# Optimization experiments

Hardware: AMD Instinct MI355X
Metric: run time of the kernel (lower is better)

## Reference

```python
import jax, jax.numpy as jnp
import numpy as np

B, S, D = 4, 1024, 512
E = 16            # num_skills
DH = 4 * D        # expert hidden
DS = 2 * D        # shared expert hidden
TOP_K = 2
TEMP = 0.7
SHARED_SCALE = 0.25
EPS = 1e-5

def layer_norm(x, g, b):
    mu = jnp.mean(x, axis=-1, keepdims=True)
    var = jnp.mean(jnp.square(x - mu), axis=-1, keepdims=True)
    return (x - mu) * jax.lax.rsqrt(var + EPS) * g + b

def setup_inputs() -> dict:
    key = jax.random.key(0)
    ks = jax.random.split(key, 12)
    s = 0.02
    return {
        "x": jax.random.normal(ks[0], (B, S, D), jnp.float32),
        # input LayerNorm
        "ln_in_g": jnp.ones((D,), jnp.float32),
        "ln_in_b": jnp.zeros((D,), jnp.float32),
        # router Linear(D -> E)
        "router_w": jax.random.normal(ks[1], (D, E), jnp.float32) * s,
        "router_b": jnp.zeros((E,), jnp.float32),
        # experts: Linear(D->DH), SiLU, Linear(DH->D), stacked over E
        "ew1": jax.random.normal(ks[2], (E, D, DH), jnp.float32) * s,
        "eb1": jnp.zeros((E, DH), jnp.float32),
        "ew2": jax.random.normal(ks[3], (E, DH, D), jnp.float32) * s,
        "eb2": jnp.zeros((E, D), jnp.float32),
        # shared expert: Linear(D->DS), SiLU, Linear(DS->D), *0.25
        "sw1": jax.random.normal(ks[4], (D, DS), jnp.float32) * s,
        "sb1": jnp.zeros((DS,), jnp.float32),
        "sw2": jax.random.normal(ks[5], (DS, D), jnp.float32) * s,
        "sb2": jnp.zeros((D,), jnp.float32),
        # final ff: LayerNorm, Linear(D->4D), SiLU, Linear(4D->D)
        "ff_ln_g": jnp.ones((D,), jnp.float32),
        "ff_ln_b": jnp.zeros((D,), jnp.float32),
        "ff_w1": jax.random.normal(ks[6], (D, DH), jnp.float32) * s,
        "ff_b1": jnp.zeros((DH,), jnp.float32),
        "ff_w2": jax.random.normal(ks[7], (DH, D), jnp.float32) * s,
        "ff_b2": jnp.zeros((D,), jnp.float32),
    }

def reference(x, ln_in_g, ln_in_b, router_w, router_b,
              ew1, eb1, ew2, eb2, sw1, sb1, sw2, sb2,
              ff_ln_g, ff_ln_b, ff_w1, ff_b1, ff_w2, ff_b2):
    h = layer_norm(x, ln_in_g, ln_in_b)                      # [B,S,D]
    # router: softmax(Linear(h)/temperature)
    gate = jax.nn.softmax((h @ router_w + router_b) / TEMP, axis=-1)  # [B,S,E]
    vals, idx = jax.lax.top_k(gate, TOP_K)                   # [B,S,K]
    # combine weights per expert: sum_j vals_j * onehot(idx_j)
    comb = jnp.sum(jax.nn.one_hot(idx, E, dtype=h.dtype) * vals[..., None], axis=-2)  # [B,S,E]
    # all-expert forward (same math as masked loop in the original)
    eh = jax.nn.silu(jnp.einsum('bsd,edh->ebsh', h, ew1) + eb1[:, None, None, :])      # [E,B,S,DH]
    ey = jnp.einsum('ebsh,ehd->ebsd', eh, ew2) + eb2[:, None, None, :]                  # [E,B,S,D]
    mix = jnp.einsum('bse,ebsd->bsd', comb, ey)              # top-k weighted combine
    shared = (jax.nn.silu(h @ sw1 + sb1) @ sw2 + sb2) * SHARED_SCALE
    moe_out = mix + shared                                   # h after MoE
    fh = layer_norm(moe_out, ff_ln_g, ff_ln_b)
    ff_out = jax.nn.silu(fh @ ff_w1 + ff_b1) @ ff_w2 + ff_b2
    return x + moe_out + ff_out
```

## Files before the change

### kernel.cpp

```cpp
#include <hip/hip_runtime.h>
#include <stdint.h>

#define T_TOK 4096
#define DIM   512
#define NEXP  16
#define DHID  2048
#define DSH   1024
#define ROWSCAP 10240
#define MAXTILES 80

typedef __bf16 bf16x8 __attribute__((ext_vector_type(8)));
typedef float  f32x4  __attribute__((ext_vector_type(4)));
typedef unsigned short usv8 __attribute__((ext_vector_type(8)));

__device__ __forceinline__ unsigned short f2b(float f) {
  union { float f; unsigned int u; } un; un.f = f;
  unsigned int u = un.u + 0x7fffu + ((un.u >> 16) & 1u);
  return (unsigned short)(u >> 16);
}
__device__ __forceinline__ float b2f(unsigned short u) {
  union { unsigned int u; float f; } un; un.u = ((unsigned int)u) << 16; return un.f;
}

__device__ __forceinline__ void async16(void* lds, const void* gp) {
  __builtin_amdgcn_global_load_lds(
      (const __attribute__((address_space(1))) unsigned int*)gp,
      (__attribute__((address_space(3))) unsigned int*)lds, 16, 0, 0);
}

__device__ __forceinline__ void transpose64(
    const float* __restrict__ s, unsigned short* __restrict__ d, int R, int C,
    int tx, int ty, float* tile) {
  const int tid = threadIdx.x;
  const int c0 = tx * 64, r0 = ty * 64;
  const int r = tid >> 4, j4 = (tid & 15) * 4;
#pragma unroll
  for (int p = 0; p < 4; ++p) {
    const int row = r + p * 16;
    const float4 v = *(const float4*)&s[(size_t)(r0 + row) * C + c0 + j4];
    tile[row * 65 + j4 + 0] = v.x;
    tile[row * 65 + j4 + 1] = v.y;
    tile[row * 65 + j4 + 2] = v.z;
    tile[row * 65 + j4 + 3] = v.w;
  }
  __syncthreads();
  const int jj = tid & 7, cc = tid >> 3;
#pragma unroll
  for (int p = 0; p < 2; ++p) {
    const int c = cc + p * 32;
    usv8 u;
#pragma unroll
    for (int i = 0; i < 8; ++i) u[i] = f2b(tile[(jj * 8 + i) * 65 + c]);
    *(usv8*)&d[(size_t)(c0 + c) * R + r0 + jj * 8] = u;
  }
}

__global__ __launch_bounds__(256) void prep_kernel(
    const float* __restrict__ x, const float* __restrict__ g, const float* __restrict__ b,
    const float* __restrict__ rw, const float* __restrict__ rb,
    unsigned short* __restrict__ hbuf, int* __restrict__ comb_idx, float* __restrict__ comb_w,
    int* __restrict__ counts,
    const float* __restrict__ ew1, const float* __restrict__ ew2,
    const float* __restrict__ sw1, const float* __restrict__ sw2,
    const float* __restrict__ fw1, const float* __restrict__ fw2,
    unsigned short* __restrict__ ew1T, unsigned short* __restrict__ ew2T,
    unsigned short* __restrict__ sw1T, unsigned short* __restrict__ sw2T,
    unsigned short* __restrict__ fw1T, unsigned short* __restrict__ fw2T) {
  __shared__ float tile[64 * 65];
  __shared__ int hist[NEXP];
  const int id = blockIdx.x;
  if (id >= 1024) {
    int id2 = id - 1024;
    const float* s; unsigned short* d; int R, C, t, tx, ty;
    if (id2 < 4096)      { int bm = id2 >> 8; t = id2 & 255; R = 512;  C = 2048;
                           s = ew1 + (size_t)bm * R * C; d = ew1T + (size_t)bm * R * C;
                           tx = t & 31; ty = t >> 5; }
    else if (id2 < 8192) { id2 -= 4096; int bm = id2 >> 8; t = id2 & 255; R = 2048; C = 512;
                           s = ew2 + (size_t)bm * R * C; d = ew2T + (size_t)bm * R * C;
                           tx = t & 7;  ty = t >> 3; }
    else if (id2 < 8320) { t = id2 - 8192; R = 512;  C = 1024; s = sw1; d = sw1T; tx = t & 15; ty = t >> 4; }
    else if (id2 < 8448) { t = id2 - 8320; R = 1024; C = 512;  s = sw2; d = sw2T; tx = t & 7;  ty = t >> 3; }
    else if (id2 < 8704) { t = id2 - 8448; R = 512;  C = 2048; s = fw1; d = fw1T; tx = t & 31; ty = t >> 5; }
    else                 { t = id2 - 8704; R = 2048; C = 512;  s = fw2; d = fw2T; tx = t & 7;  ty = t >> 3; }
    transpose64(s, d, R, C, tx, ty, tile);
    return;
  }
  const int wid = threadIdx.x >> 6, lane = threadIdx.x & 63;
  const int t = id * 4 + wid;
  if (threadIdx.x < NEXP) hist[threadIdx.x] = 0;
  __syncthreads();

  const float4* xr = (const float4*)(x + (size_t)t * DIM);
  const float4 va = xr[lane], vb = xr[lane + 64];
  float s = (va.x + va.y) + (va.z + va.w) + ((vb.x + vb.y) + (vb.z + vb.w));
#pragma unroll
  for (int o = 32; o; o >>= 1) s += __shfl_xor(s, o, 64);
  const float mu = s * (1.f / DIM);
  float da[4] = {va.x - mu, va.y - mu, va.z - mu, va.w - mu};
  float db[4] = {vb.x - mu, vb.y - mu, vb.z - mu, vb.w - mu};
  float q = (da[0]*da[0] + da[1]*da[1]) + (da[2]*da[2] + da[3]*da[3]) +
            ((db[0]*db[0] + db[1]*db[1]) + (db[2]*db[2] + db[3]*db[3]));
#pragma unroll
  for (int o = 32; o; o >>= 1) q += __shfl_xor(q, o, 64);
  const float rs = rsqrtf(q * (1.f / DIM) + 1e-5f);
  const float4 ga = ((const float4*)g)[lane], gb4 = ((const float4*)g)[lane + 64];
  const float4 ba = ((const float4*)b)[lane], bb4 = ((const float4*)b)[lane + 64];
  float ha[4], hbv[4];
  ha[0] = da[0] * rs * ga.x + ba.x;  ha[1] = da[1] * rs * ga.y + ba.y;
  ha[2] = da[2] * rs * ga.z + ba.z;  ha[3] = da[3] * rs * ga.w + ba.w;
  hbv[0] = db[0] * rs * gb4.x + bb4.x;  hbv[1] = db[1] * rs * gb4.y + bb4.y;
  hbv[2] = db[2] * rs * gb4.z + bb4.z;  hbv[3] = db[3] * rs * gb4.w + bb4.w;
  ushort4 ua = {f2b(ha[0]), f2b(ha[1]), f2b(ha[2]), f2b(ha[3])};
  ushort4 ub = {f2b(hbv[0]), f2b(hbv[1]), f2b(hbv[2]), f2b(hbv[3])};
  ((ushort4*)(hbuf + (size_t)t * DIM))[lane] = ua;
  ((ushort4*)(hbuf + (size_t)t * DIM))[lane + 64] = ub;

  float p[NEXP];
#pragma unroll
  for (int e = 0; e < NEXP; ++e) p[e] = 0.f;
  const int col0 = lane * 4;
#pragma unroll
  for (int half = 0; half < 2; ++half) {
#pragma unroll
    for (int j = 0; j < 4; ++j) {
      const int col = half * 256 + col0 + j;
      const float hv = half ? hbv[j] : ha[j];
      const float4* wr = (const float4*)(rw + (size_t)col * NEXP);
#pragma unroll
      for (int qq = 0; qq < 4; ++qq) {
        const float4 w = wr[qq];
        p[qq * 4 + 0] += hv * w.x;  p[qq * 4 + 1] += hv * w.y;
        p[qq * 4 + 2] += hv * w.z;  p[qq * 4 + 3] += hv * w.w;
      }
    }
  }
#pragma unroll
  for (int o = 32; o; o >>= 1) {
#pragma unroll
    for (int e = 0; e < NEXP; ++e) p[e] += __shfl_xor(p[e], o, 64);
  }
  float mx = -1e30f;
#pragma unroll
  for (int e = 0; e < NEXP; ++e) {
    p[e] = (p[e] + rb[e]) * (1.f / 0.7f);
    mx = fmaxf(mx, p[e]);
  }
  float ge[NEXP], se = 0.f;
#pragma unroll
  for (int e = 0; e < NEXP; ++e) { ge[e] = __expf(p[e] - mx); se += ge[e]; }
  const float inv = 1.f / se;
  int i0 = 0; float m0 = ge[0];
#pragma unroll
  for (int e = 1; e < NEXP; ++e) if (ge[e] > m0) { m0 = ge[e]; i0 = e; }
  int i1 = -1; float m1 = -1.f;
#pragma unroll
  for (int e = 0; e < NEXP; ++e) if (e != i0 && ge[e] > m1) { m1 = ge[e]; i1 = e; }
  if (lane == 0) {
    comb_idx[t * 2] = i0; comb_idx[t * 2 + 1] = i1;
    comb_w[t * 2] = m0 * inv; comb_w[t * 2 + 1] = m1 * inv;
    atomicAdd(&hist[i0], 1); atomicAdd(&hist[i1], 1);
  }
  __syncthreads();
  if (threadIdx.x < NEXP) {
    const int c = hist[threadIdx.x];
    if (c) atomicAdd(&counts[threadIdx.x], c);
  }
}

__global__ void plan_kernel(const int* __restrict__ counts, int* __restrict__ offs,
                            int* __restrict__ fill, int* __restrict__ tiledesc) {
  if (threadIdx.x == 0) {
    int run = 0, tix = 0;
    for (int e = 0; e < NEXP; ++e) {
      offs[e] = run;
      const int nt = (counts[e] + 127) >> 7;
      for (int i = 0; i < nt; ++i) { tiledesc[tix * 2] = e; tiledesc[tix * 2 + 1] = run + i * 128; ++tix; }
      run += nt * 128;
    }
    for (; tix < MAXTILES; ++tix) { tiledesc[tix * 2] = -1; tiledesc[tix * 2 + 1] = 0; }
  }
  if (threadIdx.x < NEXP) fill[threadIdx.x] = 0;
}

__global__ __launch_bounds__(256) void scatter_kernel(
    const int* __restrict__ comb_idx, const float* __restrict__ comb_w,
    const int* __restrict__ offs, int* __restrict__ fill,
    int* __restrict__ token_list, int* __restrict__ slots) {
  const int t = blockIdx.x * 256 + threadIdx.x;
#pragma unroll
  for (int j = 0; j < 2; ++j) {
    const int e = comb_idx[t * 2 + j];
    const int p = atomicAdd(&fill[e], 1);
    const int gidx = offs[e] + p;
    token_list[gidx] = t;
    slots[t * 2 + j] = gidx;
  }
}

__global__ __launch_bounds__(256) void combine_ln_kernel(
    const unsigned short* __restrict__ eyb, const float* __restrict__ shb,
    const int* __restrict__ slots, const float* __restrict__ comb_w,
    const float* __restrict__ g, const float* __restrict__ b,
    float* __restrict__ moe, unsigned short* __restrict__ fhb) {
  const int wid = threadIdx.x >> 6, lane = threadIdx.x & 63;
  const int t = blockIdx.x * 4 + wid;
  const int s0 = slots[t * 2], s1 = slots[t * 2 + 1];
  const float w0 = comb_w[t * 2], w1 = comb_w[t * 2 + 1];
  const uint4 E0 = ((const uint4*)(eyb + (size_t)s0 * DIM))[lane];
  const uint4 E1 = ((const uint4*)(eyb + (size_t)s1 * DIM))[lane];
  const float4 sa = ((const float4*)(shb + (size_t)t * DIM))[lane * 2];
  const float4 sb = ((const float4*)(shb + (size_t)t * DIM))[lane * 2 + 1];
  const unsigned int e0[4] = {E0.x, E0.y, E0.z, E0.w};
  const unsigned int e1[4] = {E1.x, E1.y, E1.z, E1.w};
  const float shv[8] = {sa.x, sa.y, sa.z, sa.w, sb.x, sb.y, sb.z, sb.w};
  float m[8];
#pragma unroll
  for (int j = 0; j < 4; ++j) {
    m[2*j]   = w0 * b2f((unsigned short)(e0[j] & 0xffff)) + w1 * b2f((unsigned short)(e1[j] & 0xffff)) + shv[2*j];
    m[2*j+1] = w0 * b2f((unsigned short)(e0[j] >> 16))    + w1 * b2f((unsigned short)(e1[j] >> 16))    + shv[2*j+1];
  }
  float4* mo = (float4*)(moe + (size_t)t * DIM);
  mo[lane * 2]     = make_float4(m[0], m[1], m[2], m[3]);
  mo[lane * 2 + 1] = make_float4(m[4], m[5], m[6], m[7]);
  float s = 0.f;
#pragma unroll
  for (int j = 0; j < 8; ++j) s += m[j];
#pragma unroll
  for (int o = 32; o; o >>= 1) s += __shfl_xor(s, o, 64);
  const float mu = s * (1.f / DIM);
  float q = 0.f;
#pragma unroll
  for (int j = 0; j < 8; ++j) { const float d = m[j] - mu; q += d * d; }
#pragma unroll
  for (int o = 32; o; o >>= 1) q += __shfl_xor(q, o, 64);
  const float rs = rsqrtf(q * (1.f / DIM) + 1e-5f);
  const float4 ga = ((const float4*)g)[lane * 2], gb4 = ((const float4*)g)[lane * 2 + 1];
  const float4 ba = ((const float4*)b)[lane * 2], bb4 = ((const float4*)b)[lane * 2 + 1];
  const float gv[8] = {ga.x, ga.y, ga.z, ga.w, gb4.x, gb4.y, gb4.z, gb4.w};
  const float bv[8] = {ba.x, ba.y, ba.z, ba.w, bb4.x, bb4.y, bb4.z, bb4.w};
  ushort4 o0, o1;
  o0.x = f2b((m[0]-mu)*rs*gv[0]+bv[0]); o0.y = f2b((m[1]-mu)*rs*gv[1]+bv[1]);
  o0.z = f2b((m[2]-mu)*rs*gv[2]+bv[2]); o0.w = f2b((m[3]-mu)*rs*gv[3]+bv[3]);
  o1.x = f2b((m[4]-mu)*rs*gv[4]+bv[4]); o1.y = f2b((m[5]-mu)*rs*gv[5]+bv[5]);
  o1.z = f2b((m[6]-mu)*rs*gv[6]+bv[6]); o1.w = f2b((m[7]-mu)*rs*gv[7]+bv[7]);
  ((ushort4*)(fhb + (size_t)t * DIM))[lane * 2]     = o0;
  ((ushort4*)(fhb + (size_t)t * DIM))[lane * 2 + 1] = o1;
}

template <int MODE, bool EXPERT, int BM>
__device__ __forceinline__ void gemm_body(
    const unsigned short* __restrict__ A, int lda,
    const unsigned short* __restrict__ BT, const float* __restrict__ bias,
    int K, int N, int row0, int expert, int bn,
    const int* __restrict__ token_list,
    unsigned short* __restrict__ outA, const float* __restrict__ mix,
    const float* __restrict__ xres, float* __restrict__ outp,
    unsigned short* As, unsigned short* Bs) {
  const int tid = threadIdx.x;
  const unsigned short* Bt = BT + (size_t)expert * N * K + (size_t)bn * 128 * K;
  const float* bp = bias + (EXPERT ? expert * N : 0) + bn * 128;

  const int MA = BM / 64;
  const int r_a = tid >> 2;
  const int c8 = ((((tid & 3) - (tid >> 3)) & 3)) << 3;
  const unsigned short* arow0; const unsigned short* arow1 = nullptr;
  if (EXPERT && MODE == 0) {
    int t0 = token_list[row0 + r_a];       if (t0 < 0) t0 = 0;
    arow0 = A + (size_t)t0 * lda + c8;
    if (MA == 2) {
      int t1 = token_list[row0 + r_a + 64];  if (t1 < 0) t1 = 0;
      arow1 = A + (size_t)t1 * lda + c8;
    }
  } else {
    arow0 = A + (size_t)(row0 + r_a) * lda + c8;
    if (MA == 2) arow1 = A + (size_t)(row0 + r_a + 64) * lda + c8;
  }
  const unsigned short* brow0 = Bt + (size_t)r_a * K + c8;
  const unsigned short* brow1 = Bt + (size_t)(r_a + 64) * K + c8;

  const int lane = tid & 63, wid = tid >> 6;
  const int wm = wid & 1, wn = wid >> 1;
  const int l15 = lane & 15, qd = lane >> 4;
  const int WR = BM / 2;
  const int NA = WR / 16;

  char* asb0 = (char*)As + wid * 1024;
  char* asb1 = (char*)As + 4096 + wid * 1024;
  char* bsb0 = (char*)Bs + wid * 1024;
  char* bsb1 = (char*)Bs + 4096 + wid * 1024;

  f32x4 acc[NA][4] = {};
  const int rdsw = ((qd + (l15 >> 1)) & 3) * 8;
  const bf16x8* afp = (const bf16x8*)&As[(wm * WR + l15) * 32 + rdsw];
  const bf16x8* bfp = (const bf16x8*)&Bs[(wn * 64 + l15) * 32 + rdsw];

  for (int k0 = 0; k0 < K; k0 += 32) {
    __syncthreads();
    async16(asb0, arow0 + k0);
    if (MA == 2) async16(asb1, arow1 + k0);
    async16(bsb0, brow0 + k0);
    async16(bsb1, brow1 + k0);
    __syncthreads();
    bf16x8 af[NA], bq[4];
#pragma unroll
    for (int a = 0; a < NA; ++a) af[a] = afp[a * 64];
#pragma unroll
    for (int b2 = 0; b2 < 4; ++b2) bq[b2] = bfp[b2 * 64];
#pragma unroll
    for (int a = 0; a < NA; ++a)
#pragma unroll
      for (int b2 = 0; b2 < 4; ++b2)
        acc[a][b2] = __builtin_amdgcn_mfma_f32_16x16x32_bf16(af[a], bq[b2], acc[a][b2], 0, 0, 0);
  }

  const int mloc = wm * WR + qd * 4;
  const int nloc = wn * 64 + l15;
#pragma unroll
  for (int b2 = 0; b2 < 4; ++b2) {
    const int n = bn * 128 + nloc + b2 * 16;
    const float bv = bp[nloc + b2 * 16];
#pragma unroll
    for (int a = 0; a < NA; ++a) {
#pragma unroll
      for (int r = 0; r < 4; ++r) {
        const int m = mloc + a * 16 + r;
        const float val = acc[a][b2][r] + bv;
        if (MODE == 0) {
          const float sg = val / (1.f + __expf(-val));
          outA[(size_t)(row0 + m) * N + n] = f2b(sg);
        } else if (MODE == 1) {
          outA[(size_t)(row0 + m) * N + n] = f2b(val);
        } else if (MODE == 2) {
          outp[(size_t)(row0 + m) * DIM + n] = 0.25f * val;
        } else {
          const size_t o = (size_t)(row0 + m) * DIM + n;
          outp[o] = xres[o] + mix[o] + val;
        }
      }
    }
  }
}

__global__ __launch_bounds__(256) void gemm_g1(
    const unsigned short* __restrict__ hb,
    const unsigned short* __restrict__ ew1T, const float* __restrict__ eb1,
    const unsigned short* __restrict__ sw1T, const float* __restrict__ sb1,
    const int* __restrict__ tiledesc, const int* __restrict__ token_list,
    unsigned short* __restrict__ Abuf, unsigned short* __restrict__ Sbuf) {
  __shared__ unsigned short As[128 * 32];
  __shared__ unsigned short Bs[128 * 32];
  const int id = blockIdx.x;
  if (id < MAXTILES * 16) {
    const int by = id >> 4, bn = id & 15;
    const int expert = tiledesc[by * 2];
    if (expert < 0) return;
    const int row0 = tiledesc[by * 2 + 1];
    gemm_body<0, true, 128>(hb, DIM, ew1T, eb1, DIM, DHID, row0, expert, bn,
                            token_list, Abuf, nullptr, nullptr, nullptr, As, Bs);
  } else {
    const int id2 = id - MAXTILES * 16;
    const int by = id2 >> 3, bn = id2 & 7;
    gemm_body<0, false, 128>(hb, DIM, sw1T, sb1, DIM, DSH, by * 128, 0, bn,
                             nullptr, Sbuf, nullptr, nullptr, nullptr, As, Bs);
  }
}

__global__ __launch_bounds__(256) void gemm_g2(
    const unsigned short* __restrict__ Abuf,
    const unsigned short* __restrict__ ew2T, const float* __restrict__ eb2,
    const unsigned short* __restrict__ Sbuf,
    const unsigned short* __restrict__ sw2T, const float* __restrict__ sb2,
    const int* __restrict__ tiledesc,
    unsigned short* __restrict__ eyb, float* __restrict__ shb) {
  __shared__ unsigned short As[64 * 32];
  __shared__ unsigned short Bs[128 * 32];
  const int id = blockIdx.x;
  if (id < MAXTILES * 8) {
    const int seg = id >> 3, sub = (id >> 2) & 1, bn = id & 3;
    const int expert = tiledesc[seg * 2];
    if (expert < 0) return;
    const int row0 = tiledesc[seg * 2 + 1] + sub * 64;
    gemm_body<1, true, 64>(Abuf, DHID, ew2T, eb2, DHID, DIM, row0, expert, bn,
                           nullptr, eyb, nullptr, nullptr, nullptr, As, Bs);
  } else {
    const int id2 = id - MAXTILES * 8;
    const int by = id2 >> 2, bn = id2 & 3;
    gemm_body<2, false, 64>(Sbuf, DSH, sw2T, sb2, DSH, DIM, by * 64, 0, bn,
                            nullptr, nullptr, nullptr, nullptr, shb, As, Bs);
  }
}

__global__ __launch_bounds__(256) void gemm_ff1(
    const unsigned short* __restrict__ A,
    const unsigned short* __restrict__ BT, const float* __restrict__ bias,
    unsigned short* __restrict__ outA) {
  __shared__ unsigned short As[128 * 32];
  __shared__ unsigned short Bs[128 * 32];
  gemm_body<0, false, 128>(A, DIM, BT, bias, DIM, DHID, blockIdx.y * 128, 0, blockIdx.x,
                           nullptr, outA, nullptr, nullptr, nullptr, As, Bs);
}
__global__ __launch_bounds__(256) void gemm_ff2(
    const unsigned short* __restrict__ A,
    const unsigned short* __restrict__ BT, const float* __restrict__ bias,
    const float* __restrict__ mix, const float* __restrict__ xres,
    float* __restrict__ outp) {
  __shared__ unsigned short As[64 * 32];
  __shared__ unsigned short Bs[128 * 32];
  gemm_body<3, false, 64>(A, DHID, BT, bias, DHID, DIM, blockIdx.y * 64, 0, blockIdx.x,
                          nullptr, nullptr, mix, xres, outp, As, Bs);
}

extern "C" void kernel_launch(void* const* d_in, const int* in_sizes, int n_in,
                              void* d_out, int out_size, void* d_ws, size_t ws_size,
                              hipStream_t stream) {
  (void)in_sizes; (void)n_in; (void)out_size; (void)ws_size;
  const float* x    = (const float*)d_in[0];
  const float* lng  = (const float*)d_in[1];
  const float* lnb  = (const float*)d_in[2];
  const float* rw   = (const float*)d_in[3];
  const float* rb   = (const float*)d_in[4];
  const float* ew1  = (const float*)d_in[5];
  const float* eb1  = (const float*)d_in[6];
  const float* ew2  = (const float*)d_in[7];
  const float* eb2  = (const float*)d_in[8];
  const float* sw1  = (const float*)d_in[9];
  const float* sb1  = (const float*)d_in[10];
  const float* sw2  = (const float*)d_in[11];
  const float* sb2  = (const float*)d_in[12];
  const float* flng = (const float*)d_in[13];
  const float* flnb = (const float*)d_in[14];
  const float* fw1  = (const float*)d_in[15];
  const float* fb1  = (const float*)d_in[16];
  const float* fw2  = (const float*)d_in[17];
  const float* fb2  = (const float*)d_in[18];
  float* out = (float*)d_out;

  char* ws = (char*)d_ws;
  size_t off = 0;
  auto alloc = [&](size_t bytes) -> void* {
    void* p = ws + off;
    off += (bytes + 255) & ~(size_t)255;
    return p;
  };
  unsigned short* ew1T = (unsigned short*)alloc((size_t)NEXP * DIM * DHID * 2);
  unsigned short* ew2T = (unsigned short*)alloc((size_t)NEXP * DHID * DIM * 2);
  unsigned short* sw1T = (unsigned short*)alloc((size_t)DIM * DSH * 2);
  unsigned short* sw2T = (unsigned short*)alloc((size_t)DSH * DIM * 2);
  unsigned short* fw1T = (unsigned short*)alloc((size_t)DIM * DHID * 2);
  unsigned short* fw2T = (unsigned short*)alloc((size_t)DHID * DIM * 2);
  unsigned short* hb   = (unsigned short*)alloc((size_t)T_TOK * DIM * 2);
  unsigned short* fhb  = (unsigned short*)alloc((size_t)T_TOK * DIM * 2);
  unsigned short* Abuf = (unsigned short*)alloc((size_t)ROWSCAP * DHID * 2);
  unsigned short* Sbuf = (unsigned short*)alloc((size_t)T_TOK * DSH * 2);
  unsigned short* eyb  = (unsigned short*)alloc((size_t)ROWSCAP * DIM * 2);
  float* shb = (float*)alloc((size_t)T_TOK * DIM * 4);
  float* moe = (float*)alloc((size_t)T_TOK * DIM * 4);
  int*   comb_idx = (int*)alloc((size_t)T_TOK * 2 * 4);
  float* comb_w   = (float*)alloc((size_t)T_TOK * 2 * 4);
  int*   slots    = (int*)alloc((size_t)T_TOK * 2 * 4);
  int* counts   = (int*)alloc(64);
  int* offs     = (int*)alloc(64);
  int* fill     = (int*)alloc(64);
  int* tiledesc = (int*)alloc(MAXTILES * 2 * 4);
  int* token_list = (int*)alloc((size_t)ROWSCAP * 4);

  hipMemsetAsync(counts, 0, 64, stream);
  hipMemsetAsync(token_list, 0xFF, (size_t)ROWSCAP * 4, stream);

  prep_kernel<<<9984, 256, 0, stream>>>(x, lng, lnb, rw, rb, hb, comb_idx, comb_w, counts,
                                        ew1, ew2, sw1, sw2, fw1, fw2,
                                        ew1T, ew2T, sw1T, sw2T, fw1T, fw2T);
  plan_kernel<<<1, 64, 0, stream>>>(counts, offs, fill, tiledesc);
  scatter_kernel<<<T_TOK / 256, 256, 0, stream>>>(comb_idx, comb_w, offs, fill, token_list, slots);

  gemm_g1<<<MAXTILES * 16 + 256, 256, 0, stream>>>(hb, ew1T, eb1, sw1T, sb1,
                                                   tiledesc, token_list, Abuf, Sbuf);
  gemm_g2<<<MAXTILES * 8 + 256, 256, 0, stream>>>(Abuf, ew2T, eb2, Sbuf, sw2T, sb2,
                                                  tiledesc, eyb, shb);
  combine_ln_kernel<<<T_TOK / 4, 256, 0, stream>>>(eyb, shb, slots, comb_w, flng, flnb, moe, fhb);
  gemm_ff1<<<dim3(DHID / 128, T_TOK / 128), 256, 0, stream>>>(fhb, fw1T, fb1, Abuf);
  gemm_ff2<<<dim3(DIM / 128, T_TOK / 64), 256, 0, stream>>>(Abuf, fw2T, fb2, moe, x, out);
}
```

Measured before the change: 400.7 us.

## Double K-step per barrier pair and reorder block mapping to share weight tiles

The GEMM main loop now stages two 32-wide K chunks into LDS per iteration, so there is one pair of __syncthreads per 64 K instead of per 32, and each wave issues twice the MFMAs between barriers. LDS arrays double in size to hold both chunks. Block index decoding is also changed so consecutive blocks share the same weight column tile (bn) and walk over row tiles, which should improve L2 reuse of weights. The larger LDS footprint may reduce occupancy.

Measured after the change: 409.2 us. 2.1% more time.

```diff
diff --git a/kernel.cpp b/kernel.cpp
--- a/kernel.cpp
+++ b/kernel.cpp
@@ -261,6 +261,7 @@
   const float* bp = bias + (EXPERT ? expert * N : 0) + bn * 128;
 
   const int MA = BM / 64;
+  const int ACH = BM * 32;
   const int r_a = tid >> 2;
   const int c8 = ((((tid & 3) - (tid >> 3)) & 3)) << 3;
   const unsigned short* arow0; const unsigned short* arow1 = nullptr;
@@ -285,7 +286,7 @@
   const int NA = WR / 16;
 
   char* asb0 = (char*)As + wid * 1024;
-  char* asb1 = (char*)As + 4096 + wid * 1024;
+  char* asb1 = (char*)As + (ACH / 2) * 2 + wid * 1024;
   char* bsb0 = (char*)Bs + wid * 1024;
   char* bsb1 = (char*)Bs + 4096 + wid * 1024;
 
@@ -294,23 +295,32 @@
   const bf16x8* afp = (const bf16x8*)&As[(wm * WR + l15) * 32 + rdsw];
   const bf16x8* bfp = (const bf16x8*)&Bs[(wn * 64 + l15) * 32 + rdsw];
 
-  for (int k0 = 0; k0 < K; k0 += 32) {
+  for (int k0 = 0; k0 < K; k0 += 64) {
     __syncthreads();
     async16(asb0, arow0 + k0);
     if (MA == 2) async16(asb1, arow1 + k0);
     async16(bsb0, brow0 + k0);
     async16(bsb1, brow1 + k0);
+    async16(asb0 + ACH * 2, arow0 + k0 + 32);
+    if (MA == 2) async16(asb1 + ACH * 2, arow1 + k0 + 32);
+    async16(bsb0 + 8192, brow0 + k0 + 32);
+    async16(bsb1 + 8192, brow1 + k0 + 32);
     __syncthreads();
-    bf16x8 af[NA], bq[4];
-#pragma unroll
-    for (int a = 0; a < NA; ++a) af[a] = afp[a * 64];
-#pragma unroll
-    for (int b2 = 0; b2 < 4; ++b2) bq[b2] = bfp[b2 * 64];
-#pragma unroll
-    for (int a = 0; a < NA; ++a)
-#pragma unroll
-      for (int b2 = 0; b2 < 4; ++b2)
-        acc[a][b2] = __builtin_amdgcn_mfma_f32_16x16x32_bf16(af[a], bq[b2], acc[a][b2], 0, 0, 0);
+#pragma unroll
+    for (int ch = 0; ch < 2; ++ch) {
+      const bf16x8* afc = (const bf16x8*)((const char*)afp + ch * ACH * 2);
+      const bf16x8* bfc = (const bf16x8*)((const char*)bfp + ch * 8192);
+      bf16x8 af[NA], bq[4];
+#pragma unroll
+      for (int a = 0; a < NA; ++a) af[a] = afc[a * 64];
+#pragma unroll
+      for (int b2 = 0; b2 < 4; ++b2) bq[b2] = bfc[b2 * 64];
+#pragma unroll
+      for (int a = 0; a < NA; ++a)
+#pragma unroll
+        for (int b2 = 0; b2 < 4; ++b2)
+          acc[a][b2] = __builtin_amdgcn_mfma_f32_16x16x32_bf16(af[a], bq[b2], acc[a][b2], 0, 0, 0);
+    }
   }
 
   const int mloc = wm * WR + qd * 4;
@@ -347,11 +357,11 @@
     const unsigned short* __restrict__ sw1T, const float* __restrict__ sb1,
     const int* __restrict__ tiledesc, const int* __restrict__ token_list,
     unsigned short* __restrict__ Abuf, unsigned short* __restrict__ Sbuf) {
-  __shared__ unsigned short As[128 * 32];
-  __shared__ unsigned short Bs[128 * 32];
+  __shared__ unsigned short As[128 * 64];
+  __shared__ unsigned short Bs[128 * 64];
   const int id = blockIdx.x;
   if (id < MAXTILES * 16) {
-    const int by = id >> 4, bn = id & 15;
+    const int bn = id / MAXTILES, by = id % MAXTILES;
     const int expert = tiledesc[by * 2];
     if (expert < 0) return;
     const int row0 = tiledesc[by * 2 + 1];
@@ -359,7 +369,7 @@
                             token_list, Abuf, nullptr, nullptr, nullptr, As, Bs);
   } else {
     const int id2 = id - MAXTILES * 16;
-    const int by = id2 >> 3, bn = id2 & 7;
+    const int bn = id2 >> 5, by = id2 & 31;
     gemm_body<0, false, 128>(hb, DIM, sw1T, sb1, DIM, DSH, by * 128, 0, bn,
                              nullptr, Sbuf, nullptr, nullptr, nullptr, As, Bs);
   }
@@ -372,11 +382,12 @@
     const unsigned short* __restrict__ sw2T, const float* __restrict__ sb2,
     const int* __restrict__ tiledesc,
     unsigned short* __restrict__ eyb, float* __restrict__ shb) {
-  __shared__ unsigned short As[64 * 32];
-  __shared__ unsigned short Bs[128 * 32];
+  __shared__ unsigned short As[64 * 64];
+  __shared__ unsigned short Bs[128 * 64];
   const int id = blockIdx.x;
   if (id < MAXTILES * 8) {
-    const int seg = id >> 3, sub = (id >> 2) & 1, bn = id & 3;
+    const int bn = id / (MAXTILES * 2), rest = id % (MAXTILES * 2);
+    const int seg = rest >> 1, sub = rest & 1;
     const int expert = tiledesc[seg * 2];
     if (expert < 0) return;
     const int row0 = tiledesc[seg * 2 + 1] + sub * 64;
@@ -384,7 +395,7 @@
                            nullptr, eyb, nullptr, nullptr, nullptr, As, Bs);
   } else {
     const int id2 = id - MAXTILES * 8;
-    const int by = id2 >> 2, bn = id2 & 3;
+    const int bn = id2 >> 6, by = id2 & 63;
     gemm_body<2, false, 64>(Sbuf, DSH, sw2T, sb2, DSH, DIM, by * 64, 0, bn,
                             nullptr, nullptr, nullptr, nullptr, shb, As, Bs);
   }
@@ -394,9 +405,9 @@
     const unsigned short* __restrict__ A,
     const unsigned short* __restrict__ BT, const float* __restrict__ bias,
     unsigned short* __restrict__ outA) {
-  __shared__ unsigned short As[128 * 32];
-  __shared__ unsigned short Bs[128 * 32];
-  gemm_body<0, false, 128>(A, DIM, BT, bias, DIM, DHID, blockIdx.y * 128, 0, blockIdx.x,
+  __shared__ unsigned short As[128 * 64];
+  __shared__ unsigned short Bs[128 * 64];
+  gemm_body<0, false, 128>(A, DIM, BT, bias, DIM, DHID, blockIdx.x * 128, 0, blockIdx.y,
                            nullptr, outA, nullptr, nullptr, nullptr, As, Bs);
 }
 __global__ __launch_bounds__(256) void gemm_ff2(
@@ -404,9 +415,9 @@
     const unsigned short* __restrict__ BT, const float* __restrict__ bias,
     const float* __restrict__ mix, const float* __restrict__ xres,
     float* __restrict__ outp) {
-  __shared__ unsigned short As[64 * 32];
-  __shared__ unsigned short Bs[128 * 32];
-  gemm_body<3, false, 64>(A, DHID, BT, bias, DHID, DIM, blockIdx.y * 64, 0, blockIdx.x,
+  __shared__ unsigned short As[64 * 64];
+  __shared__ unsigned short Bs[128 * 64];
+  gemm_body<3, false, 64>(A, DHID, BT, bias, DHID, DIM, blockIdx.x * 64, 0, blockIdx.y,
                           nullptr, nullptr, mix, xres, outp, As, Bs);
 }
 
@@ -478,6 +489,6 @@
   gemm_g2<<<MAXTILES * 8 + 256, 256, 0, stream>>>(Abuf, ew2T, eb2, Sbuf, sw2T, sb2,
                                                   tiledesc, eyb, shb);
   combine_ln_kernel<<<T_TOK / 4, 256, 0, stream>>>(eyb, shb, slots, comb_w, flng, flnb, moe, fhb);
-  gemm_ff1<<<dim3(DHID / 128, T_TOK / 128), 256, 0, stream>>>(fhb, fw1T, fb1, Abuf);
-  gemm_ff2<<<dim3(DIM / 128, T_TOK / 64), 256, 0, stream>>>(Abuf, fw2T, fb2, moe, x, out);
-}
+  gemm_ff1<<<dim3(T_TOK / 128, DHID / 128), 256, 0, stream>>>(fhb, fw1T, fb1, Abuf);
+  gemm_ff2<<<dim3(T_TOK / 64, DIM / 128), 256, 0, stream>>>(Abuf, fw2T, fb2, moe, x, out);
+}
```

## Overlap late weight transposes with first GEMM, reorder tile grids, block-local scatter

Applied to the files above, without the earlier changes.

Moves the transposes of the second-layer expert, shared and final FF weights out of the prep kernel and appends them as extra blocks of the first grouped GEMM launch. Those transposes now share the GPU with G1 compute instead of serialising ahead of it. Also reorders block-index mapping in all GEMMs so consecutive blocks share the same weight column tile, which should improve L2 reuse of weights. The scatter kernel now uses a shared-memory histogram with one global atomic per expert per block, which cuts global atomic contention but changes the order of tokens within each expert.

Result: faster. 386.6 us (-3.5%).

```diff
diff --git a/kernel.cpp b/kernel.cpp
--- a/kernel.cpp
+++ b/kernel.cpp
@@ -60,12 +60,8 @@
     const float* __restrict__ rw, const float* __restrict__ rb,
     unsigned short* __restrict__ hbuf, int* __restrict__ comb_idx, float* __restrict__ comb_w,
     int* __restrict__ counts,
-    const float* __restrict__ ew1, const float* __restrict__ ew2,
-    const float* __restrict__ sw1, const float* __restrict__ sw2,
-    const float* __restrict__ fw1, const float* __restrict__ fw2,
-    unsigned short* __restrict__ ew1T, unsigned short* __restrict__ ew2T,
-    unsigned short* __restrict__ sw1T, unsigned short* __restrict__ sw2T,
-    unsigned short* __restrict__ fw1T, unsigned short* __restrict__ fw2T) {
+    const float* __restrict__ ew1, const float* __restrict__ sw1,
+    unsigned short* __restrict__ ew1T, unsigned short* __restrict__ sw1T) {
   __shared__ float tile[64 * 65];
   __shared__ int hist[NEXP];
   const int id = blockIdx.x;
@@ -75,13 +71,7 @@
     if (id2 < 4096)      { int bm = id2 >> 8; t = id2 & 255; R = 512;  C = 2048;
                            s = ew1 + (size_t)bm * R * C; d = ew1T + (size_t)bm * R * C;
                            tx = t & 31; ty = t >> 5; }
-    else if (id2 < 8192) { id2 -= 4096; int bm = id2 >> 8; t = id2 & 255; R = 2048; C = 512;
-                           s = ew2 + (size_t)bm * R * C; d = ew2T + (size_t)bm * R * C;
-                           tx = t & 7;  ty = t >> 3; }
-    else if (id2 < 8320) { t = id2 - 8192; R = 512;  C = 1024; s = sw1; d = sw1T; tx = t & 15; ty = t >> 4; }
-    else if (id2 < 8448) { t = id2 - 8320; R = 1024; C = 512;  s = sw2; d = sw2T; tx = t & 7;  ty = t >> 3; }
-    else if (id2 < 8704) { t = id2 - 8448; R = 512;  C = 2048; s = fw1; d = fw1T; tx = t & 31; ty = t >> 5; }
-    else                 { t = id2 - 8704; R = 2048; C = 512;  s = fw2; d = fw2T; tx = t & 7;  ty = t >> 3; }
+    else                 { t = id2 - 4096; R = 512;  C = 1024; s = sw1; d = sw1T; tx = t & 15; ty = t >> 4; }
     transpose64(s, d, R, C, tx, ty, tile);
     return;
   }
@@ -183,18 +173,22 @@
 }
 
 __global__ __launch_bounds__(256) void scatter_kernel(
-    const int* __restrict__ comb_idx, const float* __restrict__ comb_w,
-    const int* __restrict__ offs, int* __restrict__ fill,
+    const int* __restrict__ comb_idx, const int* __restrict__ offs, int* __restrict__ fill,
     int* __restrict__ token_list, int* __restrict__ slots) {
+  __shared__ int hist[NEXP], base[NEXP];
+  if (threadIdx.x < NEXP) hist[threadIdx.x] = 0;
+  __syncthreads();
   const int t = blockIdx.x * 256 + threadIdx.x;
-#pragma unroll
-  for (int j = 0; j < 2; ++j) {
-    const int e = comb_idx[t * 2 + j];
-    const int p = atomicAdd(&fill[e], 1);
-    const int gidx = offs[e] + p;
-    token_list[gidx] = t;
-    slots[t * 2 + j] = gidx;
-  }
+  const int e0 = comb_idx[t * 2], e1 = comb_idx[t * 2 + 1];
+  const int r0 = atomicAdd(&hist[e0], 1);
+  const int r1 = atomicAdd(&hist[e1], 1);
+  __syncthreads();
+  if (threadIdx.x < NEXP) base[threadIdx.x] = atomicAdd(&fill[threadIdx.x], hist[threadIdx.x]);
+  __syncthreads();
+  const int g0 = offs[e0] + base[e0] + r0;
+  const int g1 = offs[e1] + base[e1] + r1;
+  token_list[g0] = t; token_list[g1] = t;
+  slots[t * 2] = g0; slots[t * 2 + 1] = g1;
 }
 
 __global__ __launch_bounds__(256) void combine_ln_kernel(
@@ -346,22 +340,37 @@
     const unsigned short* __restrict__ ew1T, const float* __restrict__ eb1,
     const unsigned short* __restrict__ sw1T, const float* __restrict__ sb1,
     const int* __restrict__ tiledesc, const int* __restrict__ token_list,
-    unsigned short* __restrict__ Abuf, unsigned short* __restrict__ Sbuf) {
-  __shared__ unsigned short As[128 * 32];
-  __shared__ unsigned short Bs[128 * 32];
+    unsigned short* __restrict__ Abuf, unsigned short* __restrict__ Sbuf,
+    const float* __restrict__ ew2, const float* __restrict__ sw2,
+    const float* __restrict__ fw1, const float* __restrict__ fw2,
+    unsigned short* __restrict__ ew2T, unsigned short* __restrict__ sw2T,
+    unsigned short* __restrict__ fw1T, unsigned short* __restrict__ fw2T) {
+  __shared__ char smem[16640];
+  unsigned short* As = (unsigned short*)smem;
+  unsigned short* Bs = (unsigned short*)(smem + 8192);
   const int id = blockIdx.x;
   if (id < MAXTILES * 16) {
-    const int by = id >> 4, bn = id & 15;
+    const int bn = id / MAXTILES, by = id % MAXTILES;
     const int expert = tiledesc[by * 2];
     if (expert < 0) return;
     const int row0 = tiledesc[by * 2 + 1];
     gemm_body<0, true, 128>(hb, DIM, ew1T, eb1, DIM, DHID, row0, expert, bn,
                             token_list, Abuf, nullptr, nullptr, nullptr, As, Bs);
-  } else {
+  } else if (id < MAXTILES * 16 + 256) {
     const int id2 = id - MAXTILES * 16;
-    const int by = id2 >> 3, bn = id2 & 7;
+    const int bn = id2 >> 5, by = id2 & 31;
     gemm_body<0, false, 128>(hb, DIM, sw1T, sb1, DIM, DSH, by * 128, 0, bn,
                              nullptr, Sbuf, nullptr, nullptr, nullptr, As, Bs);
+  } else {
+    int id2 = id - (MAXTILES * 16 + 256);
+    const float* s; unsigned short* d; int R, C, t, tx, ty;
+    if (id2 < 4096)      { int bm = id2 >> 8; t = id2 & 255; R = 2048; C = 512;
+                           s = ew2 + (size_t)bm * R * C; d = ew2T + (size_t)bm * R * C;
+                           tx = t & 7;  ty = t >> 3; }
+    else if (id2 < 4224) { t = id2 - 4096; R = 1024; C = 512;  s = sw2; d = sw2T; tx = t & 7;  ty = t >> 3; }
+    else if (id2 < 4480) { t = id2 - 4224; R = 512;  C = 2048; s = fw1; d = fw1T; tx = t & 31; ty = t >> 5; }
+    else                 { t = id2 - 4480; R = 2048; C = 512;  s = fw2; d = fw2T; tx = t & 7;  ty = t >> 3; }
+    transpose64(s, d, R, C, tx, ty, (float*)smem);
   }
 }
 
@@ -376,7 +385,8 @@
   __shared__ unsigned short Bs[128 * 32];
   const int id = blockIdx.x;
   if (id < MAXTILES * 8) {
-    const int seg = id >> 3, sub = (id >> 2) & 1, bn = id & 3;
+    const int bn = id / (MAXTILES * 2), rest = id % (MAXTILES * 2);
+    const int seg = rest >> 1, sub = rest & 1;
     const int expert = tiledesc[seg * 2];
     if (expert < 0) return;
     const int row0 = tiledesc[seg * 2 + 1] + sub * 64;
@@ -384,7 +394,7 @@
                            nullptr, eyb, nullptr, nullptr, nullptr, As, Bs);
   } else {
     const int id2 = id - MAXTILES * 8;
-    const int by = id2 >> 2, bn = id2 & 3;
+    const int bn = id2 >> 6, by = id2 & 63;
     gemm_body<2, false, 64>(Sbuf, DSH, sw2T, sb2, DSH, DIM, by * 64, 0, bn,
                             nullptr, nullptr, nullptr, nullptr, shb, As, Bs);
   }
@@ -396,7 +406,7 @@
     unsigned short* __restrict__ outA) {
   __shared__ unsigned short As[128 * 32];
   __shared__ unsigned short Bs[128 * 32];
-  gemm_body<0, false, 128>(A, DIM, BT, bias, DIM, DHID, blockIdx.y * 128, 0, blockIdx.x,
+  gemm_body<0, false, 128>(A, DIM, BT, bias, DIM, DHID, blockIdx.x * 128, 0, blockIdx.y,
                            nullptr, outA, nullptr, nullptr, nullptr, As, Bs);
 }
 __global__ __launch_bounds__(256) void gemm_ff2(
@@ -406,7 +416,7 @@
     float* __restrict__ outp) {
   __shared__ unsigned short As[64 * 32];
   __shared__ unsigned short Bs[128 * 32];
-  gemm_body<3, false, 64>(A, DHID, BT, bias, DHID, DIM, blockIdx.y * 64, 0, blockIdx.x,
+  gemm_body<3, false, 64>(A, DHID, BT, bias, DHID, DIM, blockIdx.x * 64, 0, blockIdx.y,
                           nullptr, nullptr, mix, xres, outp, As, Bs);
 }
 
@@ -467,17 +477,17 @@
   hipMemsetAsync(counts, 0, 64, stream);
   hipMemsetAsync(token_list, 0xFF, (size_t)ROWSCAP * 4, stream);
 
-  prep_kernel<<<9984, 256, 0, stream>>>(x, lng, lnb, rw, rb, hb, comb_idx, comb_w, counts,
-                                        ew1, ew2, sw1, sw2, fw1, fw2,
-                                        ew1T, ew2T, sw1T, sw2T, fw1T, fw2T);
+  prep_kernel<<<5248, 256, 0, stream>>>(x, lng, lnb, rw, rb, hb, comb_idx, comb_w, counts,
+                                        ew1, sw1, ew1T, sw1T);
   plan_kernel<<<1, 64, 0, stream>>>(counts, offs, fill, tiledesc);
-  scatter_kernel<<<T_TOK / 256, 256, 0, stream>>>(comb_idx, comb_w, offs, fill, token_list, slots);
-
-  gemm_g1<<<MAXTILES * 16 + 256, 256, 0, stream>>>(hb, ew1T, eb1, sw1T, sb1,
-                                                   tiledesc, token_list, Abuf, Sbuf);
+  scatter_kernel<<<T_TOK / 256, 256, 0, stream>>>(comb_idx, offs, fill, token_list, slots);
+
+  gemm_g1<<<MAXTILES * 16 + 256 + 4736, 256, 0, stream>>>(
+      hb, ew1T, eb1, sw1T, sb1, tiledesc, token_list, Abuf, Sbuf,
+      ew2, sw2, fw1, fw2, ew2T, sw2T, fw1T, fw2T);
   gemm_g2<<<MAXTILES * 8 + 256, 256, 0, stream>>>(Abuf, ew2T, eb2, Sbuf, sw2T, sb2,
                                                   tiledesc, eyb, shb);
   combine_ln_kernel<<<T_TOK / 4, 256, 0, stream>>>(eyb, shb, slots, comb_w, flng, flnb, moe, fhb);
-  gemm_ff1<<<dim3(DHID / 128, T_TOK / 128), 256, 0, stream>>>(fhb, fw1T, fb1, Abuf);
-  gemm_ff2<<<dim3(DIM / 128, T_TOK / 64), 256, 0, stream>>>(Abuf, fw2T, fb2, moe, x, out);
-}
+  gemm_ff1<<<dim3(T_TOK / 128, DHID / 128), 256, 0, stream>>>(fhb, fw1T, fb1, Abuf);
+  gemm_ff2<<<dim3(T_TOK / 64, DIM / 128), 256, 0, stream>>>(Abuf, fw2T, fb2, moe, x, out);
+}
```
